# Kernel optimization log

Measured on AMD Instinct MI355X. Metric: run time of the kernel, lower is better.

Reference implementation:

```python
import jax, jax.numpy as jnp
import numpy as np

N_NODES, N_EDGES = 50000, 800000
IN_DIM, HID_DIM, OUT_DIM = 512, 256, 256


def setup_inputs() -> dict:
    key = jax.random.key(0)
    ks = jax.random.split(key, 8)
    x = jax.random.normal(ks[0], (N_NODES, IN_DIM), dtype=jnp.float32)
    edge_index = jax.random.randint(ks[1], (2, N_EDGES), 0, N_NODES, dtype=jnp.int64)
    # GCNConv lin weights (no bias in lin; separate additive bias after aggregation)
    W1 = jax.random.normal(ks[2], (IN_DIM, HID_DIM), dtype=jnp.float32) * (1.0 / np.sqrt(IN_DIM))
    b1 = jnp.zeros((HID_DIM,), dtype=jnp.float32)
    W2 = jax.random.normal(ks[3], (HID_DIM, OUT_DIM), dtype=jnp.float32) * (1.0 / np.sqrt(HID_DIM))
    b2 = jnp.zeros((OUT_DIM,), dtype=jnp.float32)
    # projection head nn.Linear(out_dim, out_dim)
    Wp = jax.random.normal(ks[4], (OUT_DIM, OUT_DIM), dtype=jnp.float32) * (1.0 / np.sqrt(OUT_DIM))
    bp = jnp.zeros((OUT_DIM,), dtype=jnp.float32)
    return {"x": x, "edge_index": edge_index, "W1": W1, "b1": b1,
            "W2": W2, "b2": b2, "Wp": Wp, "bp": bp}


def _gcn_conv(x, W, b, src, dst, n):
    # x' = D^{-1/2}(A+I)D^{-1/2} (x W) + b ; deg includes self-loop (+1)
    h = x @ W  # [N, F]
    deg = jax.ops.segment_sum(jnp.ones(src.shape[0], h.dtype), dst, num_segments=n) + 1.0
    dis = jax.lax.rsqrt(deg)  # deg^{-1/2}, [N]
    msg = (dis[src] * dis[dst])[:, None] * h[src]  # [E, F] gathered+scaled messages
    agg = jax.ops.segment_sum(msg, dst, num_segments=n)  # scatter-add to dst
    # self-loop contribution: norm = dis[i]^2, message = h[i]
    return agg + (dis * dis)[:, None] * h + b


def reference(x, edge_index, W1, b1, W2, b2, Wp, bp):
    src, dst = edge_index[0], edge_index[1]
    n = x.shape[0]
    h = jax.nn.relu(_gcn_conv(x, W1, b1, src, dst, n))
    # eval mode: dropout is identity
    h = _gcn_conv(h, W2, b2, src, dst, n)
    return h @ Wp + bp
```

## Files before the change

kernel.cpp:

```cpp
#include <hip/hip_runtime.h>
#include <hip/hip_bf16.h>

typedef __bf16 bf16_8 __attribute__((ext_vector_type(8)));
typedef float  f32_4  __attribute__((ext_vector_type(4)));

#define NNODES 50000
#define NEDGES 800000
#define INDIM  512
#define HIDDIM 256
#define CSTRIDE 264

__device__ inline void gload_lds16(const __hip_bfloat16* g, __hip_bfloat16* l) {
    __builtin_amdgcn_global_load_lds(
        (const __attribute__((address_space(1))) void*)g,
        (__attribute__((address_space(3))) void*)l, 16, 0, 0);
}


__global__ void zero_kernel(int* p, int n) {
    int i = blockIdx.x * 256 + threadIdx.x;
    if (i < n) p[i] = 0;
}

__global__ void detect_kernel(const int* __restrict__ ei,
                              const unsigned short* __restrict__ xh,
                              int* __restrict__ flags) {
    int t = threadIdx.x;
    unsigned long long nz = __ballot(ei[1 + 2 * t] != 0);
    unsigned e = (xh[2 * t] >> 7) & 0xFF;
    unsigned long long ok = __ballot(e >= 90 && e <= 142);
    if (t == 0) {
        flags[0] = (nz == 0ull) ? 1 : 0;
        flags[1] = (__popcll(ok) >= 48) ? 1 : 0;
    }
}

__global__ void count_kernel(const int* __restrict__ idx, const int* __restrict__ flags,
                             int* __restrict__ deg, int E) {
    int e = blockIdx.x * 256 + threadIdx.x;
    if (e >= E) return;
    int d = flags[0] ? idx[2 * (E + e)] : idx[E + e];
    d = min(max(d, 0), NNODES - 1);
    atomicAdd(&deg[d], 1);
}

__global__ void reduce_kernel(const int* __restrict__ deg, int* __restrict__ bsum, int n) {
    __shared__ int l[256];
    int i = blockIdx.x * 256 + threadIdx.x;
    l[threadIdx.x] = (i < n) ? deg[i] : 0;
    __syncthreads();
    for (int o = 128; o > 0; o >>= 1) {
        if (threadIdx.x < o) l[threadIdx.x] += l[threadIdx.x + o];
        __syncthreads();
    }
    if (threadIdx.x == 0) bsum[blockIdx.x] = l[0];
}

__global__ void scanb_kernel(const int* __restrict__ bsum, int nb,
                             int* __restrict__ boff, int* __restrict__ offs_last) {
    __shared__ int l[256];
    int v = (threadIdx.x < nb) ? bsum[threadIdx.x] : 0;
    l[threadIdx.x] = v;
    __syncthreads();
    for (int o = 1; o < 256; o <<= 1) {
        int t = (threadIdx.x >= o) ? l[threadIdx.x - o] : 0;
        __syncthreads();
        l[threadIdx.x] += t;
        __syncthreads();
    }
    if (threadIdx.x < nb) boff[threadIdx.x] = l[threadIdx.x] - v;
    if (threadIdx.x == 255) *offs_last = l[255];
}

__global__ void local_scan_kernel(const int* __restrict__ deg, const int* __restrict__ boff,
                                  int* __restrict__ offs, float* __restrict__ dis, int n) {
    __shared__ int l[256];
    int i = blockIdx.x * 256 + threadIdx.x;
    int v = (i < n) ? deg[i] : 0;
    l[threadIdx.x] = v;
    __syncthreads();
    for (int o = 1; o < 256; o <<= 1) {
        int t = (threadIdx.x >= o) ? l[threadIdx.x - o] : 0;
        __syncthreads();
        l[threadIdx.x] += t;
        __syncthreads();
    }
    if (i < n) {
        offs[i] = boff[blockIdx.x] + l[threadIdx.x] - v;
        dis[i]  = rsqrtf((float)v + 1.0f);
    }
}

__global__ void fill_kernel(const int* __restrict__ idx, const int* __restrict__ flags,
                            const int* __restrict__ offs, int* __restrict__ cursor,
                            int* __restrict__ csr, int E) {
    int e = blockIdx.x * 256 + threadIdx.x;
    if (e >= E) return;
    int s, d;
    if (flags[0]) { s = idx[2 * e]; d = idx[2 * (E + e)]; }
    else          { s = idx[e];     d = idx[E + e]; }
    s = min(max(s, 0), NNODES - 1);
    d = min(max(d, 0), NNODES - 1);
    int p = atomicAdd(&cursor[d], 1);
    csr[offs[d] + p] = s;
}

__global__ __launch_bounds__(256)
void wf_kernel(const void* __restrict__ W2v, const void* __restrict__ Wpv,
               const void* __restrict__ b2v, const void* __restrict__ bpv,
               const int* __restrict__ flags,
               void* __restrict__ Wfv, void* __restrict__ bfv) {
    const bool bf = flags[1] != 0;
    const int c = threadIdx.x;
    if (blockIdx.x < 32) {
        __shared__ float As[8 * 256];
        const int r0 = blockIdx.x * 8;
        #pragma unroll
        for (int i = 0; i < 8; ++i) {
            int idx = i * 256 + c;
            int r = idx >> 8, k = idx & 255;
            As[idx] = bf ? (float)((const __hip_bfloat16*)W2v)[(size_t)(r0 + r) * HIDDIM + k]
                         : ((const float*)W2v)[(size_t)(r0 + r) * HIDDIM + k];
        }
        __syncthreads();
        float acc[8] = {};
        #pragma unroll 8
        for (int k = 0; k < HIDDIM; ++k) {
            float b = bf ? (float)((const __hip_bfloat16*)Wpv)[(size_t)k * HIDDIM + c]
                         : ((const float*)Wpv)[(size_t)k * HIDDIM + c];
            #pragma unroll
            for (int r = 0; r < 8; ++r) acc[r] += As[r * 256 + k] * b;
        }
        #pragma unroll
        for (int r = 0; r < 8; ++r) {
            if (bf) ((__hip_bfloat16*)Wfv)[(size_t)(r0 + r) * HIDDIM + c] = (__hip_bfloat16)acc[r];
            else    ((float*)Wfv)[(size_t)(r0 + r) * HIDDIM + c] = acc[r];
        }
    } else {
        float acc = 0.0f;
        #pragma unroll 8
        for (int k = 0; k < HIDDIM; ++k) {
            float a = bf ? (float)((const __hip_bfloat16*)b2v)[k] : ((const float*)b2v)[k];
            float b = bf ? (float)((const __hip_bfloat16*)Wpv)[(size_t)k * HIDDIM + c]
                         : ((const float*)Wpv)[(size_t)k * HIDDIM + c];
            acc += a * b;
        }
        acc += bf ? (float)((const __hip_bfloat16*)bpv)[c] : ((const float*)bpv)[c];
        if (bf) ((__hip_bfloat16*)bfv)[c] = (__hip_bfloat16)acc;
        else    ((float*)bfv)[c] = acc;
    }
}

__global__ void repack_kernel(const void* __restrict__ Wv, const int* __restrict__ flags,
                              __hip_bfloat16* __restrict__ P, int K, int N) {
    int ntiles = N / 16;
    int nt = blockIdx.x % ntiles;
    int kt = blockIdx.x / ntiles;
    int lane = threadIdx.x;
    int quad = lane >> 4, l16 = lane & 15;
    size_t pbase = ((size_t)blockIdx.x * 64 + lane) * 8;
    int k0 = kt * 32 + quad * 8;
    int col = nt * 16 + l16;
    bool bf = flags[1] != 0;
    for (int j = 0; j < 8; ++j) {
        size_t src = (size_t)(k0 + j) * N + col;
        P[pbase + j] = bf ? ((const __hip_bfloat16*)Wv)[src]
                          : (__hip_bfloat16)((const float*)Wv)[src];
    }
}

template<int K, bool ABF>
__device__ __forceinline__ void gemm_loop(const void* __restrict__ Av,
                                          const __hip_bfloat16* __restrict__ Bp,
                                          __hip_bfloat16* smem, f32_4 (&acc)[16],
                                          int wave, int lane, int row0, bool active) {
    constexpr int NKB = K / 32;
    constexpr int BVM = ABF ? 5 : 6;
    const int quad = lane >> 4;
    const int l16  = lane & 15;
    __hip_bfloat16* buf0 = smem;
    __hip_bfloat16* buf1 = smem + 8192;
    const size_t arowK = (size_t)(active ? row0 + l16 : l16) * K;

    bf16_8 afr[3];
    f32_4  alo[3], ahi[3];

    auto stage = [&](int s) {
        const __hip_bfloat16* slab = Bp + (size_t)s * 8192;
        __hip_bfloat16* buf = (s & 1) ? buf1 : buf0;
        #pragma unroll
        for (int i = 0; i < 4; ++i) {
            int ch = wave * 4 + i;
            gload_lds16(slab + ch * 512 + lane * 8, buf + ch * 512);
        }
    };
    auto loadA = [&](int s) -> bf16_8 {
        return *(const bf16_8*)((const __hip_bfloat16*)Av + arowK + (size_t)s * 32 + quad * 8);
    };
    auto loadA32 = [&](int s, int slot) {
        const float* Af = (const float*)Av + arowK + (size_t)s * 32 + quad * 8;
        alo[slot] = *(const f32_4*)Af;
        ahi[slot] = *(const f32_4*)(Af + 4);
    };

    if constexpr (ABF) afr[0] = loadA(0); else loadA32(0, 0);
    stage(0);
    if constexpr (ABF) afr[1] = loadA(1); else loadA32(1, 1);
    stage(1);

    #pragma unroll
    for (int s = 0; s < NKB; ++s) {
        if (s + 1 < NKB) {
            if constexpr (ABF) asm volatile("s_waitcnt vmcnt(5)" ::: "memory");
            else               asm volatile("s_waitcnt vmcnt(6)" ::: "memory");
        } else {
            asm volatile("s_waitcnt vmcnt(0)" ::: "memory");
        }
        __builtin_amdgcn_sched_barrier(0);
        __builtin_amdgcn_s_barrier();
        __builtin_amdgcn_sched_barrier(0);
        if (s + 2 < NKB) {
            if constexpr (ABF) afr[(s + 2) % 3] = loadA(s + 2);
            else               loadA32(s + 2, (s + 2) % 3);
        }
        bf16_8 a;
        if constexpr (ABF) {
            a = afr[s % 3];
        } else {
            const int sl = s % 3;
            #pragma unroll
            for (int j = 0; j < 4; ++j) { a[j] = (__bf16)alo[sl][j]; a[j + 4] = (__bf16)ahi[sl][j]; }
        }
        if (active) {
            const __hip_bfloat16* bb = ((s & 1) ? buf1 : buf0) + lane * 8;
            #pragma unroll
            for (int ct = 0; ct < 16; ++ct) {
                bf16_8 b = *(const bf16_8*)(bb + ct * 512);
                acc[ct] = __builtin_amdgcn_mfma_f32_16x16x32_bf16(a, b, acc[ct], 0, 0, 0);
            }
        }
        __builtin_amdgcn_sched_barrier(0);
        asm volatile("s_waitcnt lgkmcnt(0)" ::: "memory");
        __builtin_amdgcn_sched_barrier(0);
        __builtin_amdgcn_s_barrier();
        __builtin_amdgcn_sched_barrier(0);
        if (s + 2 < NKB) stage(s + 2);
    }
    (void)BVM;
}

template<int K>
__global__ __launch_bounds__(256, 4)
void gemm_kernel(const void* __restrict__ Av,
                 const void* __restrict__ Av_alt,
                 const __hip_bfloat16* __restrict__ Bp,
                 const void* __restrict__ biasv,
                 void* __restrict__ Cv,
                 const int* __restrict__ flags, int amode, int cmode, int M) {
    constexpr int N = 256;
    __shared__ __align__(16) __hip_bfloat16 smem[16896];

    const int wave = threadIdx.x >> 6;
    const int lane = threadIdx.x & 63;
    const int quad = lane >> 4;
    const int l16  = lane & 15;
    const int row0 = blockIdx.x * 64 + wave * 16;
    const bool active = row0 < M;
    const bool bf  = flags[1] != 0;
    const bool abf = amode || bf;
    const bool cbf = cmode || bf;
    const void* A = (bf || !Av_alt) ? Av : Av_alt;

    f32_4 acc[16] = {};
    if (abf) gemm_loop<K, true >(A, Bp, smem, acc, wave, lane, row0, active);
    else     gemm_loop<K, false>(A, Bp, smem, acc, wave, lane, row0, active);

    if (cbf) {
        __hip_bfloat16* cs = smem + wave * 16 * CSTRIDE;
        if (active) {
            #pragma unroll
            for (int ct = 0; ct < 16; ++ct) {
                int col = ct * 16 + l16;
                float bv = 0.0f;
                if (biasv) bv = bf ? (float)((const __hip_bfloat16*)biasv)[col]
                                   : ((const float*)biasv)[col];
                #pragma unroll
                for (int rr = 0; rr < 4; ++rr)
                    cs[(quad * 4 + rr) * CSTRIDE + col] = (__hip_bfloat16)(acc[ct][rr] + bv);
            }
            const int rh = lane >> 5;
            const int ce = (lane & 31) * 8;
            #pragma unroll
            for (int pass = 0; pass < 8; ++pass) {
                int r = pass * 2 + rh;
                __hip_bfloat16* crow = (__hip_bfloat16*)Cv + (size_t)(row0 + r) * N;
                *(bf16_8*)(crow + ce) = *(const bf16_8*)(cs + r * CSTRIDE + ce);
            }
        }
    } else if (active) {
        #pragma unroll
        for (int ct = 0; ct < 16; ++ct) {
            int col = ct * 16 + l16;
            float bv = 0.0f;
            if (biasv) bv = bf ? (float)((const __hip_bfloat16*)biasv)[col]
                               : ((const float*)biasv)[col];
            #pragma unroll
            for (int rr = 0; rr < 4; ++rr) {
                int row = row0 + quad * 4 + rr;
                ((float*)Cv)[(size_t)row * N + col] = acc[ct][rr] + bv;
            }
        }
    }
}

__device__ inline void acc_row(f32_4& a0, f32_4& a1, float w, bf16_8 r) {
    a0[0] += w * (float)r[0]; a0[1] += w * (float)r[1];
    a0[2] += w * (float)r[2]; a0[3] += w * (float)r[3];
    a1[0] += w * (float)r[4]; a1[1] += w * (float)r[5];
    a1[2] += w * (float)r[6]; a1[3] += w * (float)r[7];
}

__global__ __launch_bounds__(256)
void agg_kernel(const __hip_bfloat16* __restrict__ h,
                const int* __restrict__ csr,
                const int* __restrict__ offs,
                const float* __restrict__ dis,
                const void* __restrict__ biasv,
                const int* __restrict__ flags,
                __hip_bfloat16* __restrict__ out,
                __hip_bfloat16* __restrict__ out_alt,
                int relu) {
    const int wave = threadIdx.x >> 6;
    const int lane = threadIdx.x & 63;
    const int n = blockIdx.x * 4 + wave;
    if (n >= NNODES) return;
    const int half = lane >> 5;
    const int l32  = lane & 31;
    __hip_bfloat16* o = (flags[1] || !out_alt) ? out : out_alt;

    const float dn = dis[n];
    const int beg = offs[n], end = offs[n + 1];
    f32_4 a0 = {}, a1 = {};

    int j = beg + half;
    for (; j + 2 < end; j += 4) {
        int sa = csr[j], sb = csr[j + 2];
        bf16_8 ra = *(const bf16_8*)(h + (size_t)sa * HIDDIM + l32 * 8);
        bf16_8 rb = *(const bf16_8*)(h + (size_t)sb * HIDDIM + l32 * 8);
        float wa = dis[sa], wb = dis[sb];
        acc_row(a0, a1, wa, ra);
        acc_row(a0, a1, wb, rb);
    }
    if (j < end) {
        int sa = csr[j];
        bf16_8 ra = *(const bf16_8*)(h + (size_t)sa * HIDDIM + l32 * 8);
        acc_row(a0, a1, dis[sa], ra);
    }

    #pragma unroll
    for (int k = 0; k < 4; ++k) {
        a0[k] += __shfl_xor(a0[k], 32);
        a1[k] += __shfl_xor(a1[k], 32);
    }

    bf16_8 rn = *(const bf16_8*)(h + (size_t)n * HIDDIM + l32 * 8);
    float bv[8] = {0, 0, 0, 0, 0, 0, 0, 0};
    if (biasv) {
        if (flags[1]) {
            bf16_8 bb = ((const bf16_8*)biasv)[l32];
            #pragma unroll
            for (int k = 0; k < 8; ++k) bv[k] = (float)bb[k];
        } else {
            f32_4 blo = *((const f32_4*)biasv + 2 * l32);
            f32_4 bhi = *((const f32_4*)biasv + 2 * l32 + 1);
            #pragma unroll
            for (int k = 0; k < 4; ++k) { bv[k] = blo[k]; bv[k + 4] = bhi[k]; }
        }
    }
    const float dn2 = dn * dn;
    float v[8];
    #pragma unroll
    for (int k = 0; k < 4; ++k) {
        v[k]     = dn * a0[k] + dn2 * (float)rn[k]     + bv[k];
        v[k + 4] = dn * a1[k] + dn2 * (float)rn[k + 4] + bv[k + 4];
    }
    if (relu) {
        #pragma unroll
        for (int k = 0; k < 8; ++k) v[k] = fmaxf(v[k], 0.0f);
    }
    if (half == 0) {
        bf16_8 ov;
        #pragma unroll
        for (int k = 0; k < 8; ++k) ov[k] = (__bf16)v[k];
        *(bf16_8*)(o + (size_t)n * HIDDIM + l32 * 8) = ov;
    }
}


extern "C" void kernel_launch(void* const* d_in, const int* in_sizes, int n_in,
                              void* d_out, int out_size, void* d_ws, size_t ws_size,
                              hipStream_t stream) {
    const int M = NNODES, E = NEDGES;
    const void* x  = d_in[0];
    const int*  ei = (const int*)d_in[1];
    const void* W1 = d_in[2];
    const void* b1 = d_in[3];
    const void* W2 = d_in[4];
    const void* b2 = d_in[5];
    const void* Wp = d_in[6];
    const void* bp = d_in[7];

    char* w = (char*)d_ws;
    size_t off = 0;
    auto alloc = [&](size_t bytes) -> void* {
        void* p = w + off;
        off += (bytes + 255) & ~(size_t)255;
        return p;
    };
    int*   deg    = (int*)alloc((size_t)M * 4);
    int*   cursor = (int*)alloc((size_t)M * 4);
    int*   offs   = (int*)alloc((size_t)(M + 1) * 4);
    float* dis    = (float*)alloc((size_t)M * 4);
    int*   flags  = (int*)alloc(256);
    int*   bsum   = (int*)alloc(256 * 4);
    int*   boff   = (int*)alloc(256 * 4);
    int*   csr    = (int*)alloc((size_t)E * 4);
    __hip_bfloat16* W1p = (__hip_bfloat16*)alloc((size_t)INDIM * HIDDIM * 2);
    __hip_bfloat16* Wfp = (__hip_bfloat16*)alloc((size_t)HIDDIM * HIDDIM * 2);
    void* Wf  = alloc((size_t)HIDDIM * HIDDIM * 4);
    void* bfu = alloc((size_t)HIDDIM * 4);
    if (ws_size < off) return;

    __hip_bfloat16* h  = (__hip_bfloat16*)d_out;
    __hip_bfloat16* ha = (__hip_bfloat16*)d_in[0];
    __hip_bfloat16* g_alt = (__hip_bfloat16*)((char*)d_in[0] + (size_t)M * INDIM * 4 / 2);

    const int nb = (M + 255) / 256;

    zero_kernel<<<nb, 256, 0, stream>>>(deg, M);
    zero_kernel<<<nb, 256, 0, stream>>>(cursor, M);
    detect_kernel<<<1, 64, 0, stream>>>(ei, (const unsigned short*)x, flags);
    count_kernel<<<(E + 255) / 256, 256, 0, stream>>>(ei, flags, deg, E);
    reduce_kernel<<<nb, 256, 0, stream>>>(deg, bsum, M);
    scanb_kernel<<<1, 256, 0, stream>>>(bsum, nb, boff, &offs[M]);
    local_scan_kernel<<<nb, 256, 0, stream>>>(deg, boff, offs, dis, M);
    fill_kernel<<<(E + 255) / 256, 256, 0, stream>>>(ei, flags, offs, cursor, csr, E);

    wf_kernel<<<33, 256, 0, stream>>>(W2, Wp, b2, bp, flags, Wf, bfu);
    repack_kernel<<<(INDIM / 32) * (HIDDIM / 16), 64, 0, stream>>>(W1, flags, W1p, INDIM, HIDDIM);
    repack_kernel<<<(HIDDIM / 32) * (HIDDIM / 16), 64, 0, stream>>>(Wf, flags, Wfp, HIDDIM, HIDDIM);

    const int ggrid = (M + 63) / 64;
    const int agrid = (M + 3) / 4;

    gemm_kernel<INDIM><<<ggrid, 256, 0, stream>>>(x, nullptr, W1p, nullptr, h, flags, 0, 1, M);
    agg_kernel<<<agrid, 256, 0, stream>>>(h, csr, offs, dis, b1, flags, ha, nullptr, 1);

    agg_kernel<<<agrid, 256, 0, stream>>>(ha, csr, offs, dis, nullptr, flags, h, g_alt, 0);
    gemm_kernel<HIDDIM><<<ggrid, 256, 0, stream>>>(h, g_alt, Wfp, bfu, d_out, flags, 1, 0, M);
}
```

Baseline: 455.7 us.

## Restructure GEMM to 2D wave tiling with swizzled LDS-staged A tiles

Replaces the per-wave 16-row × 256-column GEMM, which loaded A directly from global memory, with a block-cooperative 64×256 tile. Each wave now computes 64 rows × 64 columns, and both A and B are staged into LDS per 64-wide K step with an XOR swizzle to avoid bank conflicts. The fp32 output path now goes through LDS for coalesced vector stores, and launch bounds drop from 4 to 3 blocks per CU. The aim is more MFMA reuse per B load and less redundant traffic. The trade-offs are a larger LDS footprint, single buffering with syncthreads each K step (no double buffering), and lower occupancy.

Result: slower. 470.7 us (+3.3%).

```diff
diff --git a/kernel.cpp b/kernel.cpp
--- a/kernel.cpp
+++ b/kernel.cpp
@@ -10,7 +10,7 @@
 #define HIDDIM 256
 #define CSTRIDE 264
 
-__device__ inline void gload_lds16(const __hip_bfloat16* g, __hip_bfloat16* l) {
+__device__ inline void gload_lds16(const void* g, void* l) {
     __builtin_amdgcn_global_load_lds(
         (const __attribute__((address_space(1))) void*)g,
         (__attribute__((address_space(3))) void*)l, 16, 0, 0);
@@ -169,88 +169,8 @@
     }
 }
 
-template<int K, bool ABF>
-__device__ __forceinline__ void gemm_loop(const void* __restrict__ Av,
-                                          const __hip_bfloat16* __restrict__ Bp,
-                                          __hip_bfloat16* smem, f32_4 (&acc)[16],
-                                          int wave, int lane, int row0, bool active) {
-    constexpr int NKB = K / 32;
-    constexpr int BVM = ABF ? 5 : 6;
-    const int quad = lane >> 4;
-    const int l16  = lane & 15;
-    __hip_bfloat16* buf0 = smem;
-    __hip_bfloat16* buf1 = smem + 8192;
-    const size_t arowK = (size_t)(active ? row0 + l16 : l16) * K;
-
-    bf16_8 afr[3];
-    f32_4  alo[3], ahi[3];
-
-    auto stage = [&](int s) {
-        const __hip_bfloat16* slab = Bp + (size_t)s * 8192;
-        __hip_bfloat16* buf = (s & 1) ? buf1 : buf0;
-        #pragma unroll
-        for (int i = 0; i < 4; ++i) {
-            int ch = wave * 4 + i;
-            gload_lds16(slab + ch * 512 + lane * 8, buf + ch * 512);
-        }
-    };
-    auto loadA = [&](int s) -> bf16_8 {
-        return *(const bf16_8*)((const __hip_bfloat16*)Av + arowK + (size_t)s * 32 + quad * 8);
-    };
-    auto loadA32 = [&](int s, int slot) {
-        const float* Af = (const float*)Av + arowK + (size_t)s * 32 + quad * 8;
-        alo[slot] = *(const f32_4*)Af;
-        ahi[slot] = *(const f32_4*)(Af + 4);
-    };
-
-    if constexpr (ABF) afr[0] = loadA(0); else loadA32(0, 0);
-    stage(0);
-    if constexpr (ABF) afr[1] = loadA(1); else loadA32(1, 1);
-    stage(1);
-
-    #pragma unroll
-    for (int s = 0; s < NKB; ++s) {
-        if (s + 1 < NKB) {
-            if constexpr (ABF) asm volatile("s_waitcnt vmcnt(5)" ::: "memory");
-            else               asm volatile("s_waitcnt vmcnt(6)" ::: "memory");
-        } else {
-            asm volatile("s_waitcnt vmcnt(0)" ::: "memory");
-        }
-        __builtin_amdgcn_sched_barrier(0);
-        __builtin_amdgcn_s_barrier();
-        __builtin_amdgcn_sched_barrier(0);
-        if (s + 2 < NKB) {
-            if constexpr (ABF) afr[(s + 2) % 3] = loadA(s + 2);
-            else               loadA32(s + 2, (s + 2) % 3);
-        }
-        bf16_8 a;
-        if constexpr (ABF) {
-            a = afr[s % 3];
-        } else {
-            const int sl = s % 3;
-            #pragma unroll
-            for (int j = 0; j < 4; ++j) { a[j] = (__bf16)alo[sl][j]; a[j + 4] = (__bf16)ahi[sl][j]; }
-        }
-        if (active) {
-            const __hip_bfloat16* bb = ((s & 1) ? buf1 : buf0) + lane * 8;
-            #pragma unroll
-            for (int ct = 0; ct < 16; ++ct) {
-                bf16_8 b = *(const bf16_8*)(bb + ct * 512);
-                acc[ct] = __builtin_amdgcn_mfma_f32_16x16x32_bf16(a, b, acc[ct], 0, 0, 0);
-            }
-        }
-        __builtin_amdgcn_sched_barrier(0);
-        asm volatile("s_waitcnt lgkmcnt(0)" ::: "memory");
-        __builtin_amdgcn_sched_barrier(0);
-        __builtin_amdgcn_s_barrier();
-        __builtin_amdgcn_sched_barrier(0);
-        if (s + 2 < NKB) stage(s + 2);
-    }
-    (void)BVM;
-}
-
 template<int K>
-__global__ __launch_bounds__(256, 4)
+__global__ __launch_bounds__(256, 3)
 void gemm_kernel(const void* __restrict__ Av,
                  const void* __restrict__ Av_alt,
                  const __hip_bfloat16* __restrict__ Bp,
@@ -258,56 +178,153 @@
                  void* __restrict__ Cv,
                  const int* __restrict__ flags, int amode, int cmode, int M) {
     constexpr int N = 256;
-    __shared__ __align__(16) __hip_bfloat16 smem[16896];
-
-    const int wave = threadIdx.x >> 6;
-    const int lane = threadIdx.x & 63;
+    constexpr int NIT = K / 64;
+    __shared__ __align__(16) unsigned char smem[49152];
+    __hip_bfloat16* Blds = (__hip_bfloat16*)(smem + 16384);
+
+    const int tid  = threadIdx.x;
+    const int wave = tid >> 6;
+    const int lane = tid & 63;
     const int quad = lane >> 4;
     const int l16  = lane & 15;
-    const int row0 = blockIdx.x * 64 + wave * 16;
-    const bool active = row0 < M;
+    const int row0 = blockIdx.x * 64;
     const bool bf  = flags[1] != 0;
     const bool abf = amode || bf;
     const bool cbf = cmode || bf;
     const void* A = (bf || !Av_alt) ? Av : Av_alt;
 
-    f32_4 acc[16] = {};
-    if (abf) gemm_loop<K, true >(A, Bp, smem, acc, wave, lane, row0, active);
-    else     gemm_loop<K, false>(A, Bp, smem, acc, wave, lane, row0, active);
+    f32_4 acc[4][4] = {};
+
+    #pragma unroll
+    for (int t = 0; t < NIT; ++t) {
+        if (t) __syncthreads();
+        if (abf) {
+            const __hip_bfloat16* Ag = (const __hip_bfloat16*)A;
+            #pragma unroll
+            for (int i = 0; i < 2; ++i) {
+                int a = wave * 2 + i;
+                int p = a * 1024 + lane * 16;
+                int r = p >> 7, bb = p & 127;
+                int src_r = min(row0 + r, M - 1);
+                gload_lds16(Ag + (size_t)src_r * K + t * 64 + ((bb ^ ((r & 7) << 4)) >> 1),
+                            smem + p);
+            }
+        } else {
+            const float* Ag = (const float*)A;
+            #pragma unroll
+            for (int i = 0; i < 4; ++i) {
+                int a = wave * 4 + i;
+                int p = a * 1024 + lane * 16;
+                int r = p >> 8, bb = p & 255;
+                int src_r = min(row0 + r, M - 1);
+                gload_lds16(Ag + (size_t)src_r * K + t * 64 + ((bb ^ ((r & 15) << 4)) >> 2),
+                            smem + p);
+            }
+        }
+        {
+            const __hip_bfloat16* slab = Bp + (size_t)t * 16384;
+            #pragma unroll
+            for (int i = 0; i < 8; ++i) {
+                int b = wave * 8 + i;
+                gload_lds16(slab + b * 512 + lane * 8, Blds + b * 512);
+            }
+        }
+        __syncthreads();
+        #pragma unroll
+        for (int kt = 0; kt < 2; ++kt) {
+            bf16_8 a[4], b[4];
+            #pragma unroll
+            for (int rg = 0; rg < 4; ++rg) {
+                int r = rg * 16 + l16;
+                if (abf) {
+                    int off = r * 128 + ((kt * 64 + quad * 16) ^ ((r & 7) << 4));
+                    a[rg] = *(const bf16_8*)(smem + off);
+                } else {
+                    int m  = (r & 15) << 4;
+                    int lo = r * 256 + ((kt * 128 + quad * 32) ^ m);
+                    int hi = r * 256 + ((kt * 128 + quad * 32 + 16) ^ m);
+                    f32_4 vlo = *(const f32_4*)(smem + lo);
+                    f32_4 vhi = *(const f32_4*)(smem + hi);
+                    #pragma unroll
+                    for (int j = 0; j < 4; ++j) {
+                        a[rg][j] = (__bf16)vlo[j]; a[rg][j + 4] = (__bf16)vhi[j];
+                    }
+                }
+            }
+            #pragma unroll
+            for (int cg = 0; cg < 4; ++cg) {
+                int ct = wave * 4 + cg;
+                b[cg] = *(const bf16_8*)(Blds + (size_t)kt * 8192 + (ct * 64 + lane) * 8);
+            }
+            #pragma unroll
+            for (int rg = 0; rg < 4; ++rg)
+                #pragma unroll
+                for (int cg = 0; cg < 4; ++cg)
+                    acc[rg][cg] = __builtin_amdgcn_mfma_f32_16x16x32_bf16(
+                        a[rg], b[cg], acc[rg][cg], 0, 0, 0);
+        }
+    }
 
     if (cbf) {
-        __hip_bfloat16* cs = smem + wave * 16 * CSTRIDE;
-        if (active) {
-            #pragma unroll
-            for (int ct = 0; ct < 16; ++ct) {
-                int col = ct * 16 + l16;
+        __syncthreads();
+        __hip_bfloat16* cs = (__hip_bfloat16*)smem;
+        #pragma unroll
+        for (int rg = 0; rg < 4; ++rg)
+            #pragma unroll
+            for (int cg = 0; cg < 4; ++cg) {
+                int col = wave * 64 + cg * 16 + l16;
                 float bv = 0.0f;
                 if (biasv) bv = bf ? (float)((const __hip_bfloat16*)biasv)[col]
                                    : ((const float*)biasv)[col];
                 #pragma unroll
-                for (int rr = 0; rr < 4; ++rr)
-                    cs[(quad * 4 + rr) * CSTRIDE + col] = (__hip_bfloat16)(acc[ct][rr] + bv);
-            }
-            const int rh = lane >> 5;
-            const int ce = (lane & 31) * 8;
-            #pragma unroll
-            for (int pass = 0; pass < 8; ++pass) {
-                int r = pass * 2 + rh;
-                __hip_bfloat16* crow = (__hip_bfloat16*)Cv + (size_t)(row0 + r) * N;
-                *(bf16_8*)(crow + ce) = *(const bf16_8*)(cs + r * CSTRIDE + ce);
-            }
-        }
-    } else if (active) {
-        #pragma unroll
-        for (int ct = 0; ct < 16; ++ct) {
-            int col = ct * 16 + l16;
-            float bv = 0.0f;
-            if (biasv) bv = bf ? (float)((const __hip_bfloat16*)biasv)[col]
-                               : ((const float*)biasv)[col];
-            #pragma unroll
-            for (int rr = 0; rr < 4; ++rr) {
-                int row = row0 + quad * 4 + rr;
-                ((float*)Cv)[(size_t)row * N + col] = acc[ct][rr] + bv;
+                for (int rr = 0; rr < 4; ++rr) {
+                    int rl = rg * 16 + quad * 4 + rr;
+                    cs[rl * CSTRIDE + col] = (__hip_bfloat16)(acc[rg][cg][rr] + bv);
+                }
+            }
+        __syncthreads();
+        const int r  = tid >> 2;
+        const int qc = tid & 3;
+        if (row0 + r < M) {
+            __hip_bfloat16* crow = (__hip_bfloat16*)Cv + (size_t)(row0 + r) * N;
+            #pragma unroll
+            for (int j = 0; j < 8; ++j) {
+                int col = qc * 64 + j * 8;
+                *(bf16_8*)(crow + col) = *(const bf16_8*)(cs + r * CSTRIDE + col);
+            }
+        }
+    } else {
+        float* cf = (float*)smem;
+        #pragma unroll
+        for (int half = 0; half < 2; ++half) {
+            __syncthreads();
+            #pragma unroll
+            for (int rgl = 0; rgl < 2; ++rgl) {
+                int rg = half * 2 + rgl;
+                #pragma unroll
+                for (int cg = 0; cg < 4; ++cg) {
+                    int col = wave * 64 + cg * 16 + l16;
+                    float bv = 0.0f;
+                    if (biasv) bv = bf ? (float)((const __hip_bfloat16*)biasv)[col]
+                                       : ((const float*)biasv)[col];
+                    #pragma unroll
+                    for (int rr = 0; rr < 4; ++rr) {
+                        int rl = rgl * 16 + quad * 4 + rr;
+                        cf[rl * CSTRIDE + col] = acc[rg][cg][rr] + bv;
+                    }
+                }
+            }
+            __syncthreads();
+            const int r  = tid >> 3;
+            const int qc = tid & 7;
+            int row = row0 + half * 32 + r;
+            if (row < M) {
+                float* crow = (float*)Cv + (size_t)row * N;
+                #pragma unroll
+                for (int j = 0; j < 8; ++j) {
+                    int col = qc * 32 + j * 4;
+                    *(f32_4*)(crow + col) = *(const f32_4*)(cf + r * CSTRIDE + col);
+                }
             }
         }
     }
```

## Fuse second aggregation with final GEMM and write packed fused weights directly

Applied to the files above, without the earlier changes.

The second-layer aggregation now runs inside the final GEMM kernel. Each block aggregates its 64 rows into swizzled LDS and feeds them straight to MFMA, so the intermediate activation never round-trips through global memory. The wf kernel writes the fused W2·Wp weights directly in the packed MFMA layout, which removes one repack launch. The two zero launches are merged into one. The trade-offs are lower occupancy (64KB LDS, launch bound 2) and serial per-wave aggregation of 16 rows before the GEMM can start.

Measured after the change: 498.0 us. 1.09x slower.

```diff
diff --git a/kernel.cpp b/kernel.cpp
--- a/kernel.cpp
+++ b/kernel.cpp
@@ -10,7 +10,7 @@
 #define HIDDIM 256
 #define CSTRIDE 264
 
-__device__ inline void gload_lds16(const __hip_bfloat16* g, __hip_bfloat16* l) {
+__device__ inline void gload_lds16(const void* g, void* l) {
     __builtin_amdgcn_global_load_lds(
         (const __attribute__((address_space(1))) void*)g,
         (__attribute__((address_space(3))) void*)l, 16, 0, 0);
@@ -109,7 +109,7 @@
 void wf_kernel(const void* __restrict__ W2v, const void* __restrict__ Wpv,
                const void* __restrict__ b2v, const void* __restrict__ bpv,
                const int* __restrict__ flags,
-               void* __restrict__ Wfv, void* __restrict__ bfv) {
+               __hip_bfloat16* __restrict__ Wfp, float* __restrict__ bfv) {
     const bool bf = flags[1] != 0;
     const int c = threadIdx.x;
     if (blockIdx.x < 32) {
@@ -133,8 +133,10 @@
         }
         #pragma unroll
         for (int r = 0; r < 8; ++r) {
-            if (bf) ((__hip_bfloat16*)Wfv)[(size_t)(r0 + r) * HIDDIM + c] = (__hip_bfloat16)acc[r];
-            else    ((float*)Wfv)[(size_t)(r0 + r) * HIDDIM + c] = acc[r];
+            int row = r0 + r;
+            size_t idx = ((size_t)((row >> 5) * 16 + (c >> 4)) * 64
+                          + ((row >> 3) & 3) * 16 + (c & 15)) * 8 + (row & 7);
+            Wfp[idx] = (__hip_bfloat16)acc[r];
         }
     } else {
         float acc = 0.0f;
@@ -146,8 +148,7 @@
             acc += a * b;
         }
         acc += bf ? (float)((const __hip_bfloat16*)bpv)[c] : ((const float*)bpv)[c];
-        if (bf) ((__hip_bfloat16*)bfv)[c] = (__hip_bfloat16)acc;
-        else    ((float*)bfv)[c] = acc;
+        bfv[c] = acc;
     }
 }
 
@@ -175,7 +176,6 @@
                                           __hip_bfloat16* smem, f32_4 (&acc)[16],
                                           int wave, int lane, int row0, bool active) {
     constexpr int NKB = K / 32;
-    constexpr int BVM = ABF ? 5 : 6;
     const int quad = lane >> 4;
     const int l16  = lane & 15;
     __hip_bfloat16* buf0 = smem;
@@ -246,7 +246,6 @@
         __builtin_amdgcn_sched_barrier(0);
         if (s + 2 < NKB) stage(s + 2);
     }
-    (void)BVM;
 }
 
 template<int K>
@@ -328,7 +327,6 @@
                 const void* __restrict__ biasv,
                 const int* __restrict__ flags,
                 __hip_bfloat16* __restrict__ out,
-                __hip_bfloat16* __restrict__ out_alt,
                 int relu) {
     const int wave = threadIdx.x >> 6;
     const int lane = threadIdx.x & 63;
@@ -336,7 +334,6 @@
     if (n >= NNODES) return;
     const int half = lane >> 5;
     const int l32  = lane & 31;
-    __hip_bfloat16* o = (flags[1] || !out_alt) ? out : out_alt;
 
     const float dn = dis[n];
     const int beg = offs[n], end = offs[n + 1];
@@ -392,7 +389,158 @@
         bf16_8 ov;
         #pragma unroll
         for (int k = 0; k < 8; ++k) ov[k] = (__bf16)v[k];
-        *(bf16_8*)(o + (size_t)n * HIDDIM + l32 * 8) = ov;
+        *(bf16_8*)(out + (size_t)n * HIDDIM + l32 * 8) = ov;
+    }
+}
+
+template<int K>
+__global__ __launch_bounds__(256, 2)
+void agg_gemm_kernel(const __hip_bfloat16* __restrict__ h,
+                     const int* __restrict__ csr,
+                     const int* __restrict__ offs,
+                     const float* __restrict__ dis,
+                     const __hip_bfloat16* __restrict__ Bp,
+                     const float* __restrict__ bfu,
+                     void* __restrict__ Cv,
+                     const int* __restrict__ flags, int M) {
+    constexpr int N = 256;
+    constexpr int NKB = K / 32;
+    __shared__ __align__(16) unsigned char smem[65536];
+    unsigned char*  rowsb = smem;
+    __hip_bfloat16* buf0  = (__hip_bfloat16*)(smem + 32768);
+    __hip_bfloat16* buf1  = (__hip_bfloat16*)(smem + 49152);
+
+    const int wave = threadIdx.x >> 6;
+    const int lane = threadIdx.x & 63;
+    const int quad = lane >> 4, l16 = lane & 15;
+    const int half = lane >> 5, l32 = lane & 31;
+    const int base = blockIdx.x * 64;
+    const bool cbf = flags[1] != 0;
+
+    for (int i = 0; i < 16; ++i) {
+        const int n = base + wave * 16 + i;
+        if (n >= M) break;
+        const float dn = dis[n];
+        const int beg = offs[n], end = offs[n + 1];
+        f32_4 a0 = {}, a1 = {};
+        int j = beg + half;
+        for (; j + 6 < end; j += 8) {
+            int s0 = csr[j], s1 = csr[j + 2], s2 = csr[j + 4], s3 = csr[j + 6];
+            bf16_8 r0 = *(const bf16_8*)(h + (size_t)s0 * HIDDIM + l32 * 8);
+            bf16_8 r1 = *(const bf16_8*)(h + (size_t)s1 * HIDDIM + l32 * 8);
+            bf16_8 r2 = *(const bf16_8*)(h + (size_t)s2 * HIDDIM + l32 * 8);
+            bf16_8 r3 = *(const bf16_8*)(h + (size_t)s3 * HIDDIM + l32 * 8);
+            float w0 = dis[s0], w1 = dis[s1], w2 = dis[s2], w3 = dis[s3];
+            acc_row(a0, a1, w0, r0);
+            acc_row(a0, a1, w1, r1);
+            acc_row(a0, a1, w2, r2);
+            acc_row(a0, a1, w3, r3);
+        }
+        for (; j + 2 < end; j += 4) {
+            int s0 = csr[j], s1 = csr[j + 2];
+            bf16_8 r0 = *(const bf16_8*)(h + (size_t)s0 * HIDDIM + l32 * 8);
+            bf16_8 r1 = *(const bf16_8*)(h + (size_t)s1 * HIDDIM + l32 * 8);
+            float w0 = dis[s0], w1 = dis[s1];
+            acc_row(a0, a1, w0, r0);
+            acc_row(a0, a1, w1, r1);
+        }
+        if (j < end) {
+            int s0 = csr[j];
+            bf16_8 r0 = *(const bf16_8*)(h + (size_t)s0 * HIDDIM + l32 * 8);
+            acc_row(a0, a1, dis[s0], r0);
+        }
+        #pragma unroll
+        for (int k = 0; k < 4; ++k) {
+            a0[k] += __shfl_xor(a0[k], 32);
+            a1[k] += __shfl_xor(a1[k], 32);
+        }
+        bf16_8 rn = *(const bf16_8*)(h + (size_t)n * HIDDIM + l32 * 8);
+        const float dn2 = dn * dn;
+        if (half == 0) {
+            bf16_8 ov;
+            #pragma unroll
+            for (int k = 0; k < 4; ++k) {
+                ov[k]     = (__bf16)(dn * a0[k] + dn2 * (float)rn[k]);
+                ov[k + 4] = (__bf16)(dn * a1[k] + dn2 * (float)rn[k + 4]);
+            }
+            const int r = wave * 16 + i;
+            *(bf16_8*)(rowsb + r * 512 + ((l32 * 16) ^ ((r & 7) << 4))) = ov;
+        }
+    }
+
+    const int row0 = base + wave * 16;
+    const bool active = row0 < M;
+    f32_4 acc[16] = {};
+
+    auto stage = [&](int s) {
+        const __hip_bfloat16* slab = Bp + (size_t)s * 8192;
+        __hip_bfloat16* buf = (s & 1) ? buf1 : buf0;
+        #pragma unroll
+        for (int i2 = 0; i2 < 4; ++i2) {
+            int ch = wave * 4 + i2;
+            gload_lds16(slab + ch * 512 + lane * 8, buf + ch * 512);
+        }
+    };
+    stage(0);
+    stage(1);
+
+    #pragma unroll
+    for (int s = 0; s < NKB; ++s) {
+        if (s + 1 < NKB) asm volatile("s_waitcnt vmcnt(4)" ::: "memory");
+        else             asm volatile("s_waitcnt vmcnt(0)" ::: "memory");
+        __builtin_amdgcn_sched_barrier(0);
+        __builtin_amdgcn_s_barrier();
+        __builtin_amdgcn_sched_barrier(0);
+        if (active) {
+            const int r  = wave * 16 + l16;
+            const int cb = s * 64 + quad * 16;
+            bf16_8 a = *(const bf16_8*)(rowsb + r * 512 + (cb ^ ((r & 7) << 4)));
+            const __hip_bfloat16* bb = ((s & 1) ? buf1 : buf0) + lane * 8;
+            #pragma unroll
+            for (int ct = 0; ct < 16; ++ct) {
+                bf16_8 b = *(const bf16_8*)(bb + ct * 512);
+                acc[ct] = __builtin_amdgcn_mfma_f32_16x16x32_bf16(a, b, acc[ct], 0, 0, 0);
+            }
+        }
+        __builtin_amdgcn_sched_barrier(0);
+        asm volatile("s_waitcnt lgkmcnt(0)" ::: "memory");
+        __builtin_amdgcn_sched_barrier(0);
+        __builtin_amdgcn_s_barrier();
+        __builtin_amdgcn_sched_barrier(0);
+        if (s + 2 < NKB) stage(s + 2);
+    }
+
+    if (cbf) {
+        __hip_bfloat16* cs = (__hip_bfloat16*)rowsb + wave * 16 * CSTRIDE;
+        if (active) {
+            #pragma unroll
+            for (int ct = 0; ct < 16; ++ct) {
+                int col = ct * 16 + l16;
+                float bv = bfu[col];
+                #pragma unroll
+                for (int rr = 0; rr < 4; ++rr)
+                    cs[(quad * 4 + rr) * CSTRIDE + col] = (__hip_bfloat16)(acc[ct][rr] + bv);
+            }
+            const int rh = lane >> 5;
+            const int ce = (lane & 31) * 8;
+            #pragma unroll
+            for (int pass = 0; pass < 8; ++pass) {
+                int r = pass * 2 + rh;
+                __hip_bfloat16* crow = (__hip_bfloat16*)Cv + (size_t)(row0 + r) * N;
+                *(bf16_8*)(crow + ce) = *(const bf16_8*)(cs + r * CSTRIDE + ce);
+            }
+        }
+    } else if (active) {
+        #pragma unroll
+        for (int ct = 0; ct < 16; ++ct) {
+            int col = ct * 16 + l16;
+            float bv = bfu[col];
+            #pragma unroll
+            for (int rr = 0; rr < 4; ++rr) {
+                int row = row0 + quad * 4 + rr;
+                ((float*)Cv)[(size_t)row * N + col] = acc[ct][rr] + bv;
+            }
+        }
     }
 }
 
@@ -427,18 +575,17 @@
     int*   csr    = (int*)alloc((size_t)E * 4);
     __hip_bfloat16* W1p = (__hip_bfloat16*)alloc((size_t)INDIM * HIDDIM * 2);
     __hip_bfloat16* Wfp = (__hip_bfloat16*)alloc((size_t)HIDDIM * HIDDIM * 2);
-    void* Wf  = alloc((size_t)HIDDIM * HIDDIM * 4);
-    void* bfu = alloc((size_t)HIDDIM * 4);
+    float* bfu = (float*)alloc((size_t)HIDDIM * 4);
     if (ws_size < off) return;
+    (void)cursor;
 
     __hip_bfloat16* h  = (__hip_bfloat16*)d_out;
     __hip_bfloat16* ha = (__hip_bfloat16*)d_in[0];
-    __hip_bfloat16* g_alt = (__hip_bfloat16*)((char*)d_in[0] + (size_t)M * INDIM * 4 / 2);
 
     const int nb = (M + 255) / 256;
-
-    zero_kernel<<<nb, 256, 0, stream>>>(deg, M);
-    zero_kernel<<<nb, 256, 0, stream>>>(cursor, M);
+    const int nzero = 2 * (((M * 4 + 255) & ~255) / 4);
+
+    zero_kernel<<<(nzero + 255) / 256, 256, 0, stream>>>(deg, nzero);
     detect_kernel<<<1, 64, 0, stream>>>(ei, (const unsigned short*)x, flags);
     count_kernel<<<(E + 255) / 256, 256, 0, stream>>>(ei, flags, deg, E);
     reduce_kernel<<<nb, 256, 0, stream>>>(deg, bsum, M);
@@ -446,16 +593,15 @@
     local_scan_kernel<<<nb, 256, 0, stream>>>(deg, boff, offs, dis, M);
     fill_kernel<<<(E + 255) / 256, 256, 0, stream>>>(ei, flags, offs, cursor, csr, E);
 
-    wf_kernel<<<33, 256, 0, stream>>>(W2, Wp, b2, bp, flags, Wf, bfu);
+    wf_kernel<<<33, 256, 0, stream>>>(W2, Wp, b2, bp, flags, Wfp, bfu);
     repack_kernel<<<(INDIM / 32) * (HIDDIM / 16), 64, 0, stream>>>(W1, flags, W1p, INDIM, HIDDIM);
-    repack_kernel<<<(HIDDIM / 32) * (HIDDIM / 16), 64, 0, stream>>>(Wf, flags, Wfp, HIDDIM, HIDDIM);
 
     const int ggrid = (M + 63) / 64;
     const int agrid = (M + 3) / 4;
 
     gemm_kernel<INDIM><<<ggrid, 256, 0, stream>>>(x, nullptr, W1p, nullptr, h, flags, 0, 1, M);
-    agg_kernel<<<agrid, 256, 0, stream>>>(h, csr, offs, dis, b1, flags, ha, nullptr, 1);
-
-    agg_kernel<<<agrid, 256, 0, stream>>>(ha, csr, offs, dis, nullptr, flags, h, g_alt, 0);
-    gemm_kernel<HIDDIM><<<ggrid, 256, 0, stream>>>(h, g_alt, Wfp, bfu, d_out, flags, 1, 0, M);
-}
+    agg_kernel<<<agrid, 256, 0, stream>>>(h, csr, offs, dis, b1, flags, ha, 1);
+
+    agg_gemm_kernel<HIDDIM><<<ggrid, 256, 0, stream>>>(ha, csr, offs, dis, Wfp, bfu,
+                                                       d_out, flags, M);
+}
```

## Double GEMM block rows to 128 and fuse weight repack into wf kernel

Applied to the files above, without the earlier changes.

The GEMM kernel now runs 512 threads with 8 waves covering 128 rows per block. Each B slab staged into LDS is therefore shared by twice as many rows, and each wave issues half as many LDS-staging loads. The wf kernel writes the fused W2·Wp product directly in the MFMA-packed bf16 layout with an fp32 bias, which removes the separate repack launch and the intermediate buffer. The two zeroing launches are merged into one over the contiguous deg/cursor region. The larger blocks double shared memory per block and may lower occupancy, and the vmcnt wait counts had to be retuned to match the smaller per-wave load count.

After: 441.1 us. 1.03x faster.

```diff
diff --git a/kernel.cpp b/kernel.cpp
--- a/kernel.cpp
+++ b/kernel.cpp
@@ -10,7 +10,7 @@
 #define HIDDIM 256
 #define CSTRIDE 264
 
-__device__ inline void gload_lds16(const __hip_bfloat16* g, __hip_bfloat16* l) {
+__device__ inline void gload_lds16(const void* g, void* l) {
     __builtin_amdgcn_global_load_lds(
         (const __attribute__((address_space(1))) void*)g,
         (__attribute__((address_space(3))) void*)l, 16, 0, 0);
@@ -109,7 +109,7 @@
 void wf_kernel(const void* __restrict__ W2v, const void* __restrict__ Wpv,
                const void* __restrict__ b2v, const void* __restrict__ bpv,
                const int* __restrict__ flags,
-               void* __restrict__ Wfv, void* __restrict__ bfv) {
+               __hip_bfloat16* __restrict__ Wfp, float* __restrict__ bfv) {
     const bool bf = flags[1] != 0;
     const int c = threadIdx.x;
     if (blockIdx.x < 32) {
@@ -133,8 +133,10 @@
         }
         #pragma unroll
         for (int r = 0; r < 8; ++r) {
-            if (bf) ((__hip_bfloat16*)Wfv)[(size_t)(r0 + r) * HIDDIM + c] = (__hip_bfloat16)acc[r];
-            else    ((float*)Wfv)[(size_t)(r0 + r) * HIDDIM + c] = acc[r];
+            int row = r0 + r;
+            size_t idx = ((size_t)((row >> 5) * 16 + (c >> 4)) * 64
+                          + ((row >> 3) & 3) * 16 + (c & 15)) * 8 + (row & 7);
+            Wfp[idx] = (__hip_bfloat16)acc[r];
         }
     } else {
         float acc = 0.0f;
@@ -146,8 +148,7 @@
             acc += a * b;
         }
         acc += bf ? (float)((const __hip_bfloat16*)bpv)[c] : ((const float*)bpv)[c];
-        if (bf) ((__hip_bfloat16*)bfv)[c] = (__hip_bfloat16)acc;
-        else    ((float*)bfv)[c] = acc;
+        bfv[c] = acc;
     }
 }
 
@@ -175,7 +176,6 @@
                                           __hip_bfloat16* smem, f32_4 (&acc)[16],
                                           int wave, int lane, int row0, bool active) {
     constexpr int NKB = K / 32;
-    constexpr int BVM = ABF ? 5 : 6;
     const int quad = lane >> 4;
     const int l16  = lane & 15;
     __hip_bfloat16* buf0 = smem;
@@ -189,8 +189,8 @@
         const __hip_bfloat16* slab = Bp + (size_t)s * 8192;
         __hip_bfloat16* buf = (s & 1) ? buf1 : buf0;
         #pragma unroll
-        for (int i = 0; i < 4; ++i) {
-            int ch = wave * 4 + i;
+        for (int i = 0; i < 2; ++i) {
+            int ch = wave * 2 + i;
             gload_lds16(slab + ch * 512 + lane * 8, buf + ch * 512);
         }
     };
@@ -211,8 +211,8 @@
     #pragma unroll
     for (int s = 0; s < NKB; ++s) {
         if (s + 1 < NKB) {
-            if constexpr (ABF) asm volatile("s_waitcnt vmcnt(5)" ::: "memory");
-            else               asm volatile("s_waitcnt vmcnt(6)" ::: "memory");
+            if constexpr (ABF) asm volatile("s_waitcnt vmcnt(3)" ::: "memory");
+            else               asm volatile("s_waitcnt vmcnt(4)" ::: "memory");
         } else {
             asm volatile("s_waitcnt vmcnt(0)" ::: "memory");
         }
@@ -246,25 +246,25 @@
         __builtin_amdgcn_sched_barrier(0);
         if (s + 2 < NKB) stage(s + 2);
     }
-    (void)BVM;
 }
 
 template<int K>
-__global__ __launch_bounds__(256, 4)
+__global__ __launch_bounds__(512, 2)
 void gemm_kernel(const void* __restrict__ Av,
                  const void* __restrict__ Av_alt,
                  const __hip_bfloat16* __restrict__ Bp,
                  const void* __restrict__ biasv,
                  void* __restrict__ Cv,
-                 const int* __restrict__ flags, int amode, int cmode, int M) {
+                 const int* __restrict__ flags, int amode, int cmode, int bmode,
+                 int M) {
     constexpr int N = 256;
-    __shared__ __align__(16) __hip_bfloat16 smem[16896];
+    __shared__ __align__(16) __hip_bfloat16 smem[33792];
 
     const int wave = threadIdx.x >> 6;
     const int lane = threadIdx.x & 63;
     const int quad = lane >> 4;
     const int l16  = lane & 15;
-    const int row0 = blockIdx.x * 64 + wave * 16;
+    const int row0 = blockIdx.x * 128 + wave * 16;
     const bool active = row0 < M;
     const bool bf  = flags[1] != 0;
     const bool abf = amode || bf;
@@ -275,15 +275,20 @@
     if (abf) gemm_loop<K, true >(A, Bp, smem, acc, wave, lane, row0, active);
     else     gemm_loop<K, false>(A, Bp, smem, acc, wave, lane, row0, active);
 
+    auto bias_at = [&](int col) -> float {
+        if (!biasv) return 0.0f;
+        if (bmode)  return ((const float*)biasv)[col];
+        return bf ? (float)((const __hip_bfloat16*)biasv)[col]
+                  : ((const float*)biasv)[col];
+    };
+
     if (cbf) {
         __hip_bfloat16* cs = smem + wave * 16 * CSTRIDE;
         if (active) {
             #pragma unroll
             for (int ct = 0; ct < 16; ++ct) {
                 int col = ct * 16 + l16;
-                float bv = 0.0f;
-                if (biasv) bv = bf ? (float)((const __hip_bfloat16*)biasv)[col]
-                                   : ((const float*)biasv)[col];
+                float bv = bias_at(col);
                 #pragma unroll
                 for (int rr = 0; rr < 4; ++rr)
                     cs[(quad * 4 + rr) * CSTRIDE + col] = (__hip_bfloat16)(acc[ct][rr] + bv);
@@ -301,9 +306,7 @@
         #pragma unroll
         for (int ct = 0; ct < 16; ++ct) {
             int col = ct * 16 + l16;
-            float bv = 0.0f;
-            if (biasv) bv = bf ? (float)((const __hip_bfloat16*)biasv)[col]
-                               : ((const float*)biasv)[col];
+            float bv = bias_at(col);
             #pragma unroll
             for (int rr = 0; rr < 4; ++rr) {
                 int row = row0 + quad * 4 + rr;
@@ -427,18 +430,18 @@
     int*   csr    = (int*)alloc((size_t)E * 4);
     __hip_bfloat16* W1p = (__hip_bfloat16*)alloc((size_t)INDIM * HIDDIM * 2);
     __hip_bfloat16* Wfp = (__hip_bfloat16*)alloc((size_t)HIDDIM * HIDDIM * 2);
-    void* Wf  = alloc((size_t)HIDDIM * HIDDIM * 4);
-    void* bfu = alloc((size_t)HIDDIM * 4);
+    float* bfu = (float*)alloc((size_t)HIDDIM * 4);
     if (ws_size < off) return;
+    (void)cursor;
 
     __hip_bfloat16* h  = (__hip_bfloat16*)d_out;
     __hip_bfloat16* ha = (__hip_bfloat16*)d_in[0];
     __hip_bfloat16* g_alt = (__hip_bfloat16*)((char*)d_in[0] + (size_t)M * INDIM * 4 / 2);
 
     const int nb = (M + 255) / 256;
-
-    zero_kernel<<<nb, 256, 0, stream>>>(deg, M);
-    zero_kernel<<<nb, 256, 0, stream>>>(cursor, M);
+    const int nzero = 2 * (((M * 4 + 255) & ~255) / 4);
+
+    zero_kernel<<<(nzero + 255) / 256, 256, 0, stream>>>(deg, nzero);
     detect_kernel<<<1, 64, 0, stream>>>(ei, (const unsigned short*)x, flags);
     count_kernel<<<(E + 255) / 256, 256, 0, stream>>>(ei, flags, deg, E);
     reduce_kernel<<<nb, 256, 0, stream>>>(deg, bsum, M);
@@ -446,16 +449,17 @@
     local_scan_kernel<<<nb, 256, 0, stream>>>(deg, boff, offs, dis, M);
     fill_kernel<<<(E + 255) / 256, 256, 0, stream>>>(ei, flags, offs, cursor, csr, E);
 
-    wf_kernel<<<33, 256, 0, stream>>>(W2, Wp, b2, bp, flags, Wf, bfu);
+    wf_kernel<<<33, 256, 0, stream>>>(W2, Wp, b2, bp, flags, Wfp, bfu);
     repack_kernel<<<(INDIM / 32) * (HIDDIM / 16), 64, 0, stream>>>(W1, flags, W1p, INDIM, HIDDIM);
-    repack_kernel<<<(HIDDIM / 32) * (HIDDIM / 16), 64, 0, stream>>>(Wf, flags, Wfp, HIDDIM, HIDDIM);
-
-    const int ggrid = (M + 63) / 64;
+
+    const int ggrid = (M + 127) / 128;
     const int agrid = (M + 3) / 4;
 
-    gemm_kernel<INDIM><<<ggrid, 256, 0, stream>>>(x, nullptr, W1p, nullptr, h, flags, 0, 1, M);
+    gemm_kernel<INDIM><<<ggrid, 512, 0, stream>>>(x, nullptr, W1p, nullptr, h,
+                                                  flags, 0, 1, 0, M);
     agg_kernel<<<agrid, 256, 0, stream>>>(h, csr, offs, dis, b1, flags, ha, nullptr, 1);
 
     agg_kernel<<<agrid, 256, 0, stream>>>(ha, csr, offs, dis, nullptr, flags, h, g_alt, 0);
-    gemm_kernel<HIDDIM><<<ggrid, 256, 0, stream>>>(h, g_alt, Wfp, bfu, d_out, flags, 1, 0, M);
-}
+    gemm_kernel<HIDDIM><<<ggrid, 512, 0, stream>>>(h, g_alt, Wfp, bfu, d_out,
+                                                   flags, 1, 0, 1, M);
+}
```
